# Performance work log

Measured on AMD Instinct MI355X. Metric: run time of the kernel, lower is better.

## Reference

```python
import jax, jax.numpy as jnp
import numpy as np

BATCH_SIZE = 4096
FPC = 8  # frames per camera
DIM = 256
EPS = 1e-8


def _build_indices(B, f):
    """Replicates distmtxidxlbl: for each block and each ordered pair (row, i)
    with row < i inside the block, the logit row gathers dist[row] at columns
    [0..blk) ++ [i] ++ [blk+f..B), and the label is blk (position of the
    positive i in that gathered row)."""
    base = np.arange(B)
    anchors, cols, labels = [], [], []
    for blk in range(0, B, f):
        rest = np.concatenate([base[:blk], base[blk + f:]])  # [B - f]
        for row in range(blk, blk + f):
            for i in range(row + 1, blk + f):
                anchors.append(row)
                cols.append(np.insert(rest, blk, i))  # [B - f + 1]
                labels.append(blk)
    return (np.asarray(anchors, np.int32),
            np.stack(cols).astype(np.int32),
            np.asarray(labels, np.int32))

ANCHORS, COLS, LABELS = _build_indices(BATCH_SIZE, FPC)  # [P], [P, L], [P]


def _euclidean_distance_matrix(x):
    # Standard stable pairwise Euclidean distance (Gram-matrix form) with
    # eps substitution at exact zeros, as in utils.euclidean_distance_matrix.
    dot = x @ x.T                                  # [B, B]
    sq = jnp.diagonal(dot)                         # [B]
    d2 = sq[None, :] - 2.0 * dot + sq[:, None]     # [B, B]
    d2 = jnp.maximum(d2, 0.0)
    zero = d2 == 0.0
    d = jnp.sqrt(jnp.where(zero, EPS, d2))
    return jnp.where(zero, 0.0, d)


def setup_inputs() -> dict:
    key = jax.random.key(0)
    x = jax.random.normal(key, (BATCH_SIZE, DIM), dtype=jnp.float32)
    return {"x": x}


def reference(x) -> jnp.ndarray:
    xs = jnp.squeeze(x)                                  # [B, D]
    dist = _euclidean_distance_matrix(xs)                # [B, B]
    anchors = jnp.asarray(ANCHORS)
    cols = jnp.asarray(COLS)
    labels = jnp.asarray(LABELS)
    logits = dist[anchors[:, None], cols]                # [P, L] gather
    logp = jax.nn.log_softmax(logits, axis=-1)           # [P, L]
    nll = -jnp.take_along_axis(logp, labels[:, None].astype(jnp.int32), axis=1)[:, 0]
    return jnp.mean(nll)
```

## Files before the change

kernel.cpp:

```cpp
#include <hip/hip_runtime.h>
#include <math.h>

#define BATCH 4096
#define DIM 256
#define FPC 8
#define NPAIR 14336
#define SHIFT 22.0f
#define NT 32
#define NTILE (NT * (NT + 1) / 2)
#define S_Q (127.0f / 6.0f)
#define K2 (2.0f * (6.0f / 127.0f) * (6.0f / 127.0f))
#define LOG2E 1.442695040888963f
#define NSHL2 (-(SHIFT * LOG2E))
#define PGRP 4
#define PSLOT 64

typedef int   i32x4 __attribute__((ext_vector_type(4)));

__device__ __forceinline__ void g2l16(const void* g, void* l) {
    __builtin_amdgcn_global_load_lds((__attribute__((address_space(1))) void*)(g),
                                     (__attribute__((address_space(3))) void*)(l),
                                     16, 0, 0);
}


__global__ __launch_bounds__(256) void prep_kernel(const float* __restrict__ x,
                                                   float* __restrict__ sq,
                                                   signed char* __restrict__ xq,
                                                   float* __restrict__ out) {
    int t = blockIdx.x * 256 + threadIdx.x;
    int row = t >> 6;
    int lane = t & 63;
    float4 v = ((const float4*)(x + row * DIM))[lane];
    int qx = (int)rintf(v.x * S_Q), qy = (int)rintf(v.y * S_Q);
    int qz = (int)rintf(v.z * S_Q), qw = (int)rintf(v.w * S_Q);
    qx = max(-127, min(127, qx)); qy = max(-127, min(127, qy));
    qz = max(-127, min(127, qz)); qw = max(-127, min(127, qw));
    unsigned pk = (unsigned)(qx & 255) | ((unsigned)(qy & 255) << 8) |
                  ((unsigned)(qz & 255) << 16) | ((unsigned)(qw & 255) << 24);
    ((unsigned*)(xq + (size_t)row * DIM))[lane] = pk;
    float s = v.x * v.x + v.y * v.y + v.z * v.z + v.w * v.w;
#pragma unroll
    for (int off = 32; off > 0; off >>= 1) s += __shfl_xor(s, off);
    if (lane == 0) sq[row] = s;
    if (t == 0) out[0] = 0.f;
}

__global__ __launch_bounds__(256, 2) void dist_kernel(const signed char* __restrict__ xq,
                                                      const float* __restrict__ sq,
                                                      float* __restrict__ P) {
    __shared__ signed char As[128][128];
    __shared__ signed char Bs[128][128];

    int t = blockIdx.x, bi = 0;
    while (t >= NT - bi) { t -= NT - bi; bi++; }
    const int bj = bi + t;
    const int row0 = bi * 128;
    const int col0 = bj * 128;
    const bool diagblk = (bi == bj);

    const int tid  = threadIdx.x;
    const int w    = tid >> 6;
    const int lane = tid & 63;
    const int wr   = w >> 1;
    const int wc   = w & 1;
    const int quad = lane >> 4;
    const int lcol = lane & 15;

    const int srow = lane >> 3;
    const int schk = lane & 7;
    const int gc = (schk ^ (srow & 7)) * 16;
    const int ldsoff = lane * 16;

    i32x4 acc[4][4];
#pragma unroll
    for (int i = 0; i < 4; i++)
#pragma unroll
        for (int j = 0; j < 4; j++) {
            i32x4 z = {0, 0, 0, 0};
            acc[i][j] = z;
        }

#pragma unroll
    for (int ph = 0; ph < 2; ph++) {
        const int k0 = ph * 128;
        if (ph) __syncthreads();
#pragma unroll
        for (int c = 0; c < 4; c++) {
            const int rb = w * 32 + c * 8;
            const int r  = rb + srow;
            g2l16(xq + (size_t)(row0 + r) * DIM + k0 + gc, (signed char*)&As[rb][0] + ldsoff);
            g2l16(xq + (size_t)(col0 + r) * DIM + k0 + gc, (signed char*)&Bs[rb][0] + ldsoff);
        }
        __syncthreads();

#pragma unroll
        for (int kk = 0; kk < 2; kk++) {
            const int slot = ((kk * 4 + quad) ^ (lcol & 7)) * 16;
            i32x4 a[4], bb[4];
#pragma unroll
            for (int i = 0; i < 4; i++)
                a[i] = *(const i32x4*)&As[wr * 64 + i * 16 + lcol][slot];
#pragma unroll
            for (int j = 0; j < 4; j++)
                bb[j] = *(const i32x4*)&Bs[wc * 64 + j * 16 + lcol][slot];
#pragma unroll
            for (int i = 0; i < 4; i++)
#pragma unroll
                for (int j = 0; j < 4; j++)
                    acc[i][j] = __builtin_amdgcn_mfma_i32_16x16x64_i8(a[i], bb[j], acc[i][j], 0, 0, 0);
        }
    }

    float sc2[4];
#pragma unroll
    for (int j = 0; j < 4; j++) sc2[j] = sq[col0 + wc * 64 + j * 16 + lcol];

    float cs[4] = {0.f, 0.f, 0.f, 0.f};
    const int rslot = 2 * bj + wc;
    const int cslot = 2 * bi + wr;

#pragma unroll
    for (int i = 0; i < 4; i++) {
        const int rbase = row0 + wr * 64 + i * 16 + quad * 4;
        const float4 s4 = *(const float4*)(sq + rbase);
        const float sr[4] = {s4.x, s4.y, s4.z, s4.w};
        float rs[4] = {0.f, 0.f, 0.f, 0.f};
#pragma unroll
        for (int j = 0; j < 4; j++) {
            const bool extile = diagblk && (wr * 4 + i == wc * 4 + j);
#pragma unroll
            for (int r = 0; r < 4; r++) {
                float d2 = fmaf(-(float)K2, (float)acc[i][j][r], sr[r] + sc2[j]);
                float dd = __builtin_amdgcn_sqrtf(fmaxf(d2, 0.f));
                float e = __builtin_amdgcn_exp2f(fmaf(dd, LOG2E, NSHL2));
                if (extile && (((quad * 4 + r) >> 3) == (lcol >> 3))) e = 0.f;
                rs[r] += e;
                cs[j] += e;
            }
        }
#pragma unroll
        for (int m = 1; m < 16; m <<= 1) {
#pragma unroll
            for (int r = 0; r < 4; r++) rs[r] += __shfl_xor(rs[r], m);
        }
        if (lcol == 0) {
#pragma unroll
            for (int r = 0; r < 4; r++)
                P[(size_t)(rbase + r) * PSLOT + rslot] = rs[r];
        }
    }

    if (!diagblk) {
#pragma unroll
        for (int j = 0; j < 4; j++) {
            cs[j] += __shfl_xor(cs[j], 16);
            cs[j] += __shfl_xor(cs[j], 32);
        }
        if (lane < 16) {
#pragma unroll
            for (int j = 0; j < 4; j++)
                P[(size_t)(col0 + wc * 64 + j * 16 + lane) * PSLOT + cslot] = cs[j];
        }
    }
}

__global__ __launch_bounds__(256) void pairs_kernel(const float* __restrict__ x,
                                                    const float* __restrict__ P,
                                                    float* __restrict__ out) {
    __shared__ float Srow[FPC * PGRP];
    __shared__ float wsum[4];
    const int tid = threadIdx.x;
    const int base0 = blockIdx.x * (FPC * PGRP);

    {
        const int rl = tid >> 3;
        const int l8 = tid & 7;
        const float* pr = P + (size_t)(base0 + rl) * PSLOT;
        float s2 = 0.f;
#pragma unroll
        for (int m = 0; m < 8; m++) s2 += pr[l8 + 8 * m];
        s2 += __shfl_xor(s2, 1);
        s2 += __shfl_xor(s2, 2);
        s2 += __shfl_xor(s2, 4);
        if (l8 == 0) Srow[rl] = s2;
    }
    __syncthreads();

    const int p = tid >> 3;
    const int g = tid & 7;
    int a = 0, b = 0;
    if (p < 28) {
        int q = p;
        while (q >= 7 - a) { q -= 7 - a; a++; }
        b = a + 1 + q;
    }

    float nll = 0.f;
#pragma unroll
    for (int it = 0; it < PGRP; it++) {
        if (p < 28) {
            const int base = base0 + it * FPC;
            const float4* xa  = (const float4*)(x + (size_t)(base + a) * DIM);
            const float4* xbp = (const float4*)(x + (size_t)(base + b) * DIM);
            float d2 = 0.f;
#pragma unroll
            for (int r = 0; r < 8; r++) {
                float4 va = xa[r * 8 + g], vb = xbp[r * 8 + g];
                float dx = va.x - vb.x, dy = va.y - vb.y;
                float dz = va.z - vb.z, dw = va.w - vb.w;
                d2 = fmaf(dx, dx, d2); d2 = fmaf(dy, dy, d2);
                d2 = fmaf(dz, dz, d2); d2 = fmaf(dw, dw, d2);
            }
            d2 += __shfl_xor(d2, 1);
            d2 += __shfl_xor(d2, 2);
            d2 += __shfl_xor(d2, 4);
            if (g == 0) {
                float dd = sqrtf(fmaxf(d2, 0.f));
                nll += SHIFT + __logf(Srow[it * FPC + a] + __expf(dd - SHIFT)) - dd;
            }
        }
    }
#pragma unroll
    for (int off = 1; off < 64; off <<= 1) nll += __shfl_xor(nll, off);
    if ((tid & 63) == 0) wsum[tid >> 6] = nll;
    __syncthreads();
    if (tid == 0)
        atomicAdd(out, (wsum[0] + wsum[1] + wsum[2] + wsum[3]) * (1.0f / (float)NPAIR));
}

extern "C" void kernel_launch(void* const* d_in, const int* in_sizes, int n_in,
                              void* d_out, int out_size, void* d_ws, size_t ws_size,
                              hipStream_t stream) {
    const float* x = (const float*)d_in[0];
    float* sq = (float*)d_ws;
    float* P  = sq + BATCH;
    signed char* xq = (signed char*)(P + (size_t)BATCH * PSLOT);
    float* out = (float*)d_out;

    prep_kernel<<<BATCH * 64 / 256, 256, 0, stream>>>(x, sq, xq, out);

    dist_kernel<<<NTILE, 256, 0, stream>>>(xq, sq, P);

    pairs_kernel<<<BATCH / (FPC * PGRP), 256, 0, stream>>>(x, P, out);
}
```

Baseline: 72.19 us.

## Move exact positive-pair distances into prep kernel and persist dist tiles

The fp32 positive-pair distance computation moves out of the final pairs kernel into extra blocks of the prep kernel, which write the results to a workspace buffer. The pairs kernel then only reads the sums and these distances to form the loss. The dist kernel becomes a persistent grid of 512 blocks that loop over the 528 triangular tiles. This is meant to shorten the serial tail kernel and cut launch waves, but the loop leaves a few blocks with two tiles and adds an extra barrier per tile.

Measured after the change: 74.08 us. 2.6% more time.

```diff
diff --git a/kernel.cpp b/kernel.cpp
--- a/kernel.cpp
+++ b/kernel.cpp
@@ -8,6 +8,7 @@
 #define SHIFT 22.0f
 #define NT 32
 #define NTILE (NT * (NT + 1) / 2)
+#define DGRID 512
 #define S_Q (127.0f / 6.0f)
 #define K2 (2.0f * (6.0f / 127.0f) * (6.0f / 127.0f))
 #define LOG2E 1.442695040888963f
@@ -27,23 +28,62 @@
 __global__ __launch_bounds__(256) void prep_kernel(const float* __restrict__ x,
                                                    float* __restrict__ sq,
                                                    signed char* __restrict__ xq,
+                                                   float* __restrict__ DD,
                                                    float* __restrict__ out) {
-    int t = blockIdx.x * 256 + threadIdx.x;
-    int row = t >> 6;
-    int lane = t & 63;
-    float4 v = ((const float4*)(x + row * DIM))[lane];
-    int qx = (int)rintf(v.x * S_Q), qy = (int)rintf(v.y * S_Q);
-    int qz = (int)rintf(v.z * S_Q), qw = (int)rintf(v.w * S_Q);
-    qx = max(-127, min(127, qx)); qy = max(-127, min(127, qy));
-    qz = max(-127, min(127, qz)); qw = max(-127, min(127, qw));
-    unsigned pk = (unsigned)(qx & 255) | ((unsigned)(qy & 255) << 8) |
-                  ((unsigned)(qz & 255) << 16) | ((unsigned)(qw & 255) << 24);
-    ((unsigned*)(xq + (size_t)row * DIM))[lane] = pk;
-    float s = v.x * v.x + v.y * v.y + v.z * v.z + v.w * v.w;
-#pragma unroll
-    for (int off = 32; off > 0; off >>= 1) s += __shfl_xor(s, off);
-    if (lane == 0) sq[row] = s;
-    if (t == 0) out[0] = 0.f;
+    const int tid = threadIdx.x;
+    if (blockIdx.x < BATCH / 4) {
+        int t = blockIdx.x * 256 + tid;
+        int row = t >> 6;
+        int lane = t & 63;
+        float4 v = ((const float4*)(x + row * DIM))[lane];
+        int qx = (int)rintf(v.x * S_Q), qy = (int)rintf(v.y * S_Q);
+        int qz = (int)rintf(v.z * S_Q), qw = (int)rintf(v.w * S_Q);
+        qx = max(-127, min(127, qx)); qy = max(-127, min(127, qy));
+        qz = max(-127, min(127, qz)); qw = max(-127, min(127, qw));
+        unsigned pk = (unsigned)(qx & 255) | ((unsigned)(qy & 255) << 8) |
+                      ((unsigned)(qz & 255) << 16) | ((unsigned)(qw & 255) << 24);
+        ((unsigned*)(xq + (size_t)row * DIM))[lane] = pk;
+        float s = v.x * v.x + v.y * v.y + v.z * v.z + v.w * v.w;
+#pragma unroll
+        for (int off = 32; off > 0; off >>= 1) s += __shfl_xor(s, off);
+        if (lane == 0) sq[row] = s;
+        if (t == 0) out[0] = 0.f;
+    } else {
+        const int pb = blockIdx.x - BATCH / 4;
+        const int base0 = pb * (FPC * PGRP);
+        const int p = tid >> 3;
+        const int g = tid & 7;
+        int a = 0, b = 0;
+        if (p < 28) {
+            int q = p;
+            while (q >= 7 - a) { q -= 7 - a; a++; }
+            b = a + 1 + q;
+        }
+#pragma unroll
+        for (int it = 0; it < PGRP; it++) {
+            if (p < 28) {
+                const int base = base0 + it * FPC;
+                const float4* xa  = (const float4*)(x + (size_t)(base + a) * DIM);
+                const float4* xbp = (const float4*)(x + (size_t)(base + b) * DIM);
+                float d2 = 0.f;
+#pragma unroll
+                for (int r = 0; r < 8; r++) {
+                    float4 va = xa[r * 8 + g], vb = xbp[r * 8 + g];
+                    float dx = va.x - vb.x, dy = va.y - vb.y;
+                    float dz = va.z - vb.z, dw = va.w - vb.w;
+                    d2 = fmaf(dx, dx, d2); d2 = fmaf(dy, dy, d2);
+                    d2 = fmaf(dz, dz, d2); d2 = fmaf(dw, dw, d2);
+                }
+                d2 += __shfl_xor(d2, 1);
+                d2 += __shfl_xor(d2, 2);
+                d2 += __shfl_xor(d2, 4);
+                if (g == 0) {
+                    float dd = sqrtf(fmaxf(d2, 0.f));
+                    DD[(size_t)(pb * PGRP + it) * 28 + p] = dd;
+                }
+            }
+        }
+    }
 }
 
 __global__ __launch_bounds__(256, 2) void dist_kernel(const signed char* __restrict__ xq,
@@ -51,13 +91,6 @@
                                                       float* __restrict__ P) {
     __shared__ signed char As[128][128];
     __shared__ signed char Bs[128][128];
-
-    int t = blockIdx.x, bi = 0;
-    while (t >= NT - bi) { t -= NT - bi; bi++; }
-    const int bj = bi + t;
-    const int row0 = bi * 128;
-    const int col0 = bj * 128;
-    const bool diagblk = (bi == bj);
 
     const int tid  = threadIdx.x;
     const int w    = tid >> 6;
@@ -72,100 +105,109 @@
     const int gc = (schk ^ (srow & 7)) * 16;
     const int ldsoff = lane * 16;
 
-    i32x4 acc[4][4];
-#pragma unroll
-    for (int i = 0; i < 4; i++)
-#pragma unroll
-        for (int j = 0; j < 4; j++) {
-            i32x4 z = {0, 0, 0, 0};
-            acc[i][j] = z;
-        }
-
-#pragma unroll
-    for (int ph = 0; ph < 2; ph++) {
-        const int k0 = ph * 128;
-        if (ph) __syncthreads();
-#pragma unroll
-        for (int c = 0; c < 4; c++) {
-            const int rb = w * 32 + c * 8;
-            const int r  = rb + srow;
-            g2l16(xq + (size_t)(row0 + r) * DIM + k0 + gc, (signed char*)&As[rb][0] + ldsoff);
-            g2l16(xq + (size_t)(col0 + r) * DIM + k0 + gc, (signed char*)&Bs[rb][0] + ldsoff);
-        }
-        __syncthreads();
-
-#pragma unroll
-        for (int kk = 0; kk < 2; kk++) {
-            const int slot = ((kk * 4 + quad) ^ (lcol & 7)) * 16;
-            i32x4 a[4], bb[4];
-#pragma unroll
-            for (int i = 0; i < 4; i++)
-                a[i] = *(const i32x4*)&As[wr * 64 + i * 16 + lcol][slot];
-#pragma unroll
-            for (int j = 0; j < 4; j++)
-                bb[j] = *(const i32x4*)&Bs[wc * 64 + j * 16 + lcol][slot];
-#pragma unroll
-            for (int i = 0; i < 4; i++)
+    for (int tile = blockIdx.x; tile < NTILE; tile += DGRID) {
+        int t = tile, bi = 0;
+        while (t >= NT - bi) { t -= NT - bi; bi++; }
+        const int bj = bi + t;
+        const int row0 = bi * 128;
+        const int col0 = bj * 128;
+        const bool diagblk = (bi == bj);
+
+        i32x4 acc[4][4];
+#pragma unroll
+        for (int i = 0; i < 4; i++)
+#pragma unroll
+            for (int j = 0; j < 4; j++) {
+                i32x4 z = {0, 0, 0, 0};
+                acc[i][j] = z;
+            }
+
+#pragma unroll
+        for (int ph = 0; ph < 2; ph++) {
+            const int k0 = ph * 128;
+            __syncthreads();
+#pragma unroll
+            for (int c = 0; c < 4; c++) {
+                const int rb = w * 32 + c * 8;
+                const int r  = rb + srow;
+                g2l16(xq + (size_t)(row0 + r) * DIM + k0 + gc, (signed char*)&As[rb][0] + ldsoff);
+                g2l16(xq + (size_t)(col0 + r) * DIM + k0 + gc, (signed char*)&Bs[rb][0] + ldsoff);
+            }
+            __syncthreads();
+
+#pragma unroll
+            for (int kk = 0; kk < 2; kk++) {
+                const int slot = ((kk * 4 + quad) ^ (lcol & 7)) * 16;
+                i32x4 a[4], bb[4];
+#pragma unroll
+                for (int i = 0; i < 4; i++)
+                    a[i] = *(const i32x4*)&As[wr * 64 + i * 16 + lcol][slot];
 #pragma unroll
                 for (int j = 0; j < 4; j++)
-                    acc[i][j] = __builtin_amdgcn_mfma_i32_16x16x64_i8(a[i], bb[j], acc[i][j], 0, 0, 0);
-        }
-    }
-
-    float sc2[4];
-#pragma unroll
-    for (int j = 0; j < 4; j++) sc2[j] = sq[col0 + wc * 64 + j * 16 + lcol];
-
-    float cs[4] = {0.f, 0.f, 0.f, 0.f};
-    const int rslot = 2 * bj + wc;
-    const int cslot = 2 * bi + wr;
-
-#pragma unroll
-    for (int i = 0; i < 4; i++) {
-        const int rbase = row0 + wr * 64 + i * 16 + quad * 4;
-        const float4 s4 = *(const float4*)(sq + rbase);
-        const float sr[4] = {s4.x, s4.y, s4.z, s4.w};
-        float rs[4] = {0.f, 0.f, 0.f, 0.f};
-#pragma unroll
-        for (int j = 0; j < 4; j++) {
-            const bool extile = diagblk && (wr * 4 + i == wc * 4 + j);
-#pragma unroll
-            for (int r = 0; r < 4; r++) {
-                float d2 = fmaf(-(float)K2, (float)acc[i][j][r], sr[r] + sc2[j]);
-                float dd = __builtin_amdgcn_sqrtf(fmaxf(d2, 0.f));
-                float e = __builtin_amdgcn_exp2f(fmaf(dd, LOG2E, NSHL2));
-                if (extile && (((quad * 4 + r) >> 3) == (lcol >> 3))) e = 0.f;
-                rs[r] += e;
-                cs[j] += e;
-            }
-        }
-#pragma unroll
-        for (int m = 1; m < 16; m <<= 1) {
-#pragma unroll
-            for (int r = 0; r < 4; r++) rs[r] += __shfl_xor(rs[r], m);
-        }
-        if (lcol == 0) {
-#pragma unroll
-            for (int r = 0; r < 4; r++)
-                P[(size_t)(rbase + r) * PSLOT + rslot] = rs[r];
-        }
-    }
-
-    if (!diagblk) {
-#pragma unroll
-        for (int j = 0; j < 4; j++) {
-            cs[j] += __shfl_xor(cs[j], 16);
-            cs[j] += __shfl_xor(cs[j], 32);
-        }
-        if (lane < 16) {
-#pragma unroll
-            for (int j = 0; j < 4; j++)
-                P[(size_t)(col0 + wc * 64 + j * 16 + lane) * PSLOT + cslot] = cs[j];
-        }
-    }
-}
-
-__global__ __launch_bounds__(256) void pairs_kernel(const float* __restrict__ x,
+                    bb[j] = *(const i32x4*)&Bs[wc * 64 + j * 16 + lcol][slot];
+#pragma unroll
+                for (int i = 0; i < 4; i++)
+#pragma unroll
+                    for (int j = 0; j < 4; j++)
+                        acc[i][j] = __builtin_amdgcn_mfma_i32_16x16x64_i8(a[i], bb[j], acc[i][j], 0, 0, 0);
+            }
+        }
+
+        float sc2[4];
+#pragma unroll
+        for (int j = 0; j < 4; j++) sc2[j] = sq[col0 + wc * 64 + j * 16 + lcol];
+
+        float cs[4] = {0.f, 0.f, 0.f, 0.f};
+        const int rslot = 2 * bj + wc;
+        const int cslot = 2 * bi + wr;
+
+#pragma unroll
+        for (int i = 0; i < 4; i++) {
+            const int rbase = row0 + wr * 64 + i * 16 + quad * 4;
+            const float4 s4 = *(const float4*)(sq + rbase);
+            const float sr[4] = {s4.x, s4.y, s4.z, s4.w};
+            float rs[4] = {0.f, 0.f, 0.f, 0.f};
+#pragma unroll
+            for (int j = 0; j < 4; j++) {
+                const bool extile = diagblk && (wr * 4 + i == wc * 4 + j);
+#pragma unroll
+                for (int r = 0; r < 4; r++) {
+                    float d2 = fmaf(-(float)K2, (float)acc[i][j][r], sr[r] + sc2[j]);
+                    float dd = __builtin_amdgcn_sqrtf(fmaxf(d2, 0.f));
+                    float e = __builtin_amdgcn_exp2f(fmaf(dd, LOG2E, NSHL2));
+                    if (extile && (((quad * 4 + r) >> 3) == (lcol >> 3))) e = 0.f;
+                    rs[r] += e;
+                    cs[j] += e;
+                }
+            }
+#pragma unroll
+            for (int m = 1; m < 16; m <<= 1) {
+#pragma unroll
+                for (int r = 0; r < 4; r++) rs[r] += __shfl_xor(rs[r], m);
+            }
+            if (lcol == 0) {
+#pragma unroll
+                for (int r = 0; r < 4; r++)
+                    P[(size_t)(rbase + r) * PSLOT + rslot] = rs[r];
+            }
+        }
+
+        if (!diagblk) {
+#pragma unroll
+            for (int j = 0; j < 4; j++) {
+                cs[j] += __shfl_xor(cs[j], 16);
+                cs[j] += __shfl_xor(cs[j], 32);
+            }
+            if (lane < 16) {
+#pragma unroll
+                for (int j = 0; j < 4; j++)
+                    P[(size_t)(col0 + wc * 64 + j * 16 + lane) * PSLOT + cslot] = cs[j];
+            }
+        }
+    }
+}
+
+__global__ __launch_bounds__(256) void pairs_kernel(const float* __restrict__ DD,
                                                     const float* __restrict__ P,
                                                     float* __restrict__ out) {
     __shared__ float Srow[FPC * PGRP];
@@ -187,39 +229,14 @@
     }
     __syncthreads();
 
-    const int p = tid >> 3;
-    const int g = tid & 7;
-    int a = 0, b = 0;
-    if (p < 28) {
-        int q = p;
+    float nll = 0.f;
+    if (tid < 28 * PGRP) {
+        const int gi = tid / 28;
+        const int pp = tid - gi * 28;
+        int a = 0, q = pp;
         while (q >= 7 - a) { q -= 7 - a; a++; }
-        b = a + 1 + q;
-    }
-
-    float nll = 0.f;
-#pragma unroll
-    for (int it = 0; it < PGRP; it++) {
-        if (p < 28) {
-            const int base = base0 + it * FPC;
-            const float4* xa  = (const float4*)(x + (size_t)(base + a) * DIM);
-            const float4* xbp = (const float4*)(x + (size_t)(base + b) * DIM);
-            float d2 = 0.f;
-#pragma unroll
-            for (int r = 0; r < 8; r++) {
-                float4 va = xa[r * 8 + g], vb = xbp[r * 8 + g];
-                float dx = va.x - vb.x, dy = va.y - vb.y;
-                float dz = va.z - vb.z, dw = va.w - vb.w;
-                d2 = fmaf(dx, dx, d2); d2 = fmaf(dy, dy, d2);
-                d2 = fmaf(dz, dz, d2); d2 = fmaf(dw, dw, d2);
-            }
-            d2 += __shfl_xor(d2, 1);
-            d2 += __shfl_xor(d2, 2);
-            d2 += __shfl_xor(d2, 4);
-            if (g == 0) {
-                float dd = sqrtf(fmaxf(d2, 0.f));
-                nll += SHIFT + __logf(Srow[it * FPC + a] + __expf(dd - SHIFT)) - dd;
-            }
-        }
+        const float dd = DD[(size_t)(blockIdx.x * PGRP + gi) * 28 + pp];
+        nll = SHIFT + __logf(Srow[gi * FPC + a] + __expf(dd - SHIFT)) - dd;
     }
 #pragma unroll
     for (int off = 1; off < 64; off <<= 1) nll += __shfl_xor(nll, off);
@@ -236,11 +253,12 @@
     float* sq = (float*)d_ws;
     float* P  = sq + BATCH;
     signed char* xq = (signed char*)(P + (size_t)BATCH * PSLOT);
+    float* DD = (float*)(xq + (size_t)BATCH * DIM);
     float* out = (float*)d_out;
 
-    prep_kernel<<<BATCH * 64 / 256, 256, 0, stream>>>(x, sq, xq, out);
-
-    dist_kernel<<<NTILE, 256, 0, stream>>>(xq, sq, P);
-
-    pairs_kernel<<<BATCH / (FPC * PGRP), 256, 0, stream>>>(x, P, out);
-}
+    prep_kernel<<<BATCH / 4 + BATCH / (FPC * PGRP), 256, 0, stream>>>(x, sq, xq, DD, out);
+
+    dist_kernel<<<DGRID, 256, 0, stream>>>(xq, sq, P);
+
+    pairs_kernel<<<BATCH / (FPC * PGRP), 256, 0, stream>>>(DD, P, out);
+}
```
